# Optimization experiments

Hardware: AMD Instinct MI355X
Metric: run time of the kernel (lower is better)

The kernel has to match this reference:

```python
import jax, jax.numpy as jnp
import numpy as np
from jax import lax

B, CI, CO, H, W = 2, 256, 256, 128, 128
K = 3
K2 = K * K  # 9 kernel taps
BN_EPS = 1e-5


def setup_inputs() -> dict:
    key = jax.random.key(0)
    ks = jax.random.split(key, 9)
    x = jax.random.normal(ks[0], (B, CI, H, W), jnp.float32)
    # conv_offset_mask: Conv2d(chi, 3*K2, 3, stride=1, pad=1) -> [o_y/o_x interleaved (2*K2) | mask (K2)]
    w_off = jax.random.normal(ks[1], (3 * K2, CI, K, K), jnp.float32) * 0.01
    b_off = jax.random.normal(ks[2], (3 * K2,), jnp.float32) * 0.01
    # modulated deformable conv weight/bias
    w_dcn = jax.random.normal(ks[3], (CO, CI, K, K), jnp.float32) * (1.0 / np.float32(np.sqrt(CI * K2)))
    b_dcn = jax.random.normal(ks[4], (CO,), jnp.float32) * 0.01
    # BatchNorm2d (eval-mode affine + running stats)
    gamma = jax.random.uniform(ks[5], (CO,), jnp.float32, 0.5, 1.5)
    beta = jax.random.normal(ks[6], (CO,), jnp.float32) * 0.1
    run_mean = jax.random.normal(ks[7], (CO,), jnp.float32) * 0.1
    run_var = jax.random.uniform(ks[8], (CO,), jnp.float32, 0.5, 1.5)
    return {"x": x, "w_off": w_off, "b_off": b_off, "w_dcn": w_dcn,
            "b_dcn": b_dcn, "gamma": gamma, "beta": beta,
            "run_mean": run_mean, "run_var": run_var}


def _bilinear(x, py, px):
    """Sample x [B,C,H,W] at fractional coords (py,px) [B,H,W]; zero outside."""
    Bx, C, Hx, Wx = x.shape
    y0 = jnp.floor(py)
    x0 = jnp.floor(px)
    ly = py - y0
    lx = px - x0
    xf = x.reshape(Bx, C, Hx * Wx)

    def gather(yy, xx):
        valid = ((yy >= 0) & (yy <= Hx - 1) & (xx >= 0) & (xx <= Wx - 1)).astype(x.dtype)
        yi = jnp.clip(yy, 0, Hx - 1).astype(jnp.int32)
        xi = jnp.clip(xx, 0, Wx - 1).astype(jnp.int32)
        idx = (yi * Wx + xi).reshape(Bx, 1, Hx * Wx)
        v = jnp.take_along_axis(xf, idx, axis=2).reshape(Bx, C, Hx, Wx)
        return v * valid[:, None]

    w00 = ((1 - ly) * (1 - lx))[:, None]
    w01 = ((1 - ly) * lx)[:, None]
    w10 = (ly * (1 - lx))[:, None]
    w11 = (ly * lx)[:, None]
    return (w00 * gather(y0, x0) + w01 * gather(y0, x0 + 1)
            + w10 * gather(y0 + 1, x0) + w11 * gather(y0 + 1, x0 + 1))


def _deform_conv_bn_relu(x, w_off, b_off, w_dcn, b_dcn, gamma, beta, run_mean, run_var):
    # offset/mask predictor conv (stride 1, pad 1)
    om = lax.conv_general_dilated(x, w_off, (1, 1), ((1, 1), (1, 1))) + b_off[None, :, None, None]
    dy = om[:, 0:2 * K2:2]          # [B,K2,H,W]
    dx = om[:, 1:2 * K2:2]          # [B,K2,H,W]
    mask = jax.nn.sigmoid(om[:, 2 * K2:])  # [B,K2,H,W] modulation

    hh = jnp.arange(H, dtype=x.dtype)[:, None]  # [H,1]
    ww = jnp.arange(W, dtype=x.dtype)[None, :]  # [1,W]

    out = jnp.zeros((x.shape[0], w_dcn.shape[0], H, W), x.dtype)
    for k in range(K2):  # fixed small loop over the 9 kernel taps
        i, j = k // K, k % K
        py = hh - 1 + i + dy[:, k]  # pad=1, dilation=1
        px = ww - 1 + j + dx[:, k]
        val = _bilinear(x, py, px) * mask[:, k][:, None]  # [B,CI,H,W]
        out = out + jnp.einsum('oc,bchw->bohw', w_dcn[:, :, i, j], val)
    out = out + b_dcn[None, :, None, None]

    # BatchNorm2d (eval mode) + ReLU
    inv = gamma / jnp.sqrt(run_var + BN_EPS)
    out = out * inv[None, :, None, None] + (beta - run_mean * inv)[None, :, None, None]
    return jnp.maximum(out, 0.0)


def reference(x, w_off, b_off, w_dcn, b_dcn, gamma, beta, run_mean, run_var):
    return _deform_conv_bn_relu(x, w_off, b_off, w_dcn, b_dcn, gamma, beta, run_mean, run_var)
```

## Files before the change

### kernel.cpp

```cpp
#include <hip/hip_runtime.h>
#include <math.h>

#define Bn 2
#define CIc 256
#define COc 256
#define Hh 128
#define Ww 128
#define HW (Hh*Ww)

typedef unsigned short u16;
typedef unsigned int u32;
typedef __bf16 bf16x8 __attribute__((ext_vector_type(8)));
typedef float  f32x4  __attribute__((ext_vector_type(4)));
typedef float  f32x2  __attribute__((ext_vector_type(2)));
typedef u32    u32x4v __attribute__((ext_vector_type(4)));

#define WOFP_OFF  0
#define WPACK_OFF 36864
#define SCALE_OFF 331776
#define SHIFT_OFF 332032
#define XT_OFF    332288

__device__ __forceinline__ u16 f2bf(float f) {
    u32 u = __builtin_bit_cast(u32, f);
    return (u16)((u + 0x7FFFu + ((u >> 16) & 1u)) >> 16);
}
__device__ __forceinline__ u32 pkbf(float lo, float hi) {
    __bf16 a = (__bf16)lo, b = (__bf16)hi;
    return (u32)__builtin_bit_cast(u16, a) | ((u32)__builtin_bit_cast(u16, b) << 16);
}
__device__ __forceinline__ f32x2 unpk(u32 u) {
    f32x2 r;
    r.x = __builtin_bit_cast(float, u << 16);
    r.y = __builtin_bit_cast(float, u & 0xFFFF0000u);
    return r;
}

__global__ void prep_kernel(const float* __restrict__ w_off,
                            const float* __restrict__ w_dcn,
                            const float* __restrict__ b_dcn,
                            const float* __restrict__ gamma,
                            const float* __restrict__ beta,
                            const float* __restrict__ rmean,
                            const float* __restrict__ rvar,
                            float* __restrict__ ws) {
    int tid = blockIdx.x*blockDim.x + threadIdx.x;
    int nth = gridDim.x*blockDim.x;
    u16* wofp = (u16*)(ws + WOFP_OFF);
    u16* wpk  = (u16*)(ws + WPACK_OFF);
    for (int idx = tid; idx < 9*8*32*4*8; idx += nth) {
        int j = idx & 7, kb = (idx>>3)&3, co = (idx>>5)&31, s = (idx>>10)&7, k = idx>>13;
        int ci = kb*64 + s*8 + j;
        float v = (co < 27) ? w_off[(co*CIc + ci)*9 + k] : 0.f;
        wofp[idx] = f2bf(v);
    }
    for (int idx = tid; idx < 9*8*256*4*8; idx += nth) {
        int j = idx & 7, kb = (idx>>3)&3, co = (idx>>5)&255, s = (idx>>13)&7, k = idx>>16;
        int ci = kb*64 + s*8 + j;
        wpk[idx] = f2bf(w_dcn[(co*CIc + ci)*9 + k]);
    }
    if (tid < COc) {
        float inv = gamma[tid] * rsqrtf(rvar[tid] + 1e-5f);
        ws[SCALE_OFF+tid] = inv;
        ws[SHIFT_OFF+tid] = beta[tid] - rmean[tid]*inv + b_dcn[tid]*inv;
    }
}

__global__ __launch_bounds__(256) void transpose_kernel(const float* __restrict__ x,
                                                        float* __restrict__ ws) {
    __shared__ float tile[256][33];
    int bid = blockIdx.x;
    int b   = bid >> 9;
    int pxt = bid & 511;
    const float* xb = x + (size_t)b*CIc*HW + pxt*32;
    int px = threadIdx.x & 31, cg = threadIdx.x >> 5;
    #pragma unroll 8
    for (int it = 0; it < 32; it++) {
        int ci = it*8 + cg;
        tile[ci][px] = xb[(size_t)ci*HW + px];
    }
    __syncthreads();
    int px2 = threadIdx.x >> 3, oct = threadIdx.x & 7;
    u16* xto = (u16*)(ws + XT_OFF) + (((size_t)b*HW + pxt*32 + px2) << 8);
    #pragma unroll
    for (int uu = 0; uu < 4; uu++) {
        int u = uu*8 + oct;
        int cib = (u & 3)*64 + (u >> 2)*8;
        u32x4v v;
        #pragma unroll
        for (int t = 0; t < 4; t++)
            v[t] = pkbf(tile[cib + 2*t][px2], tile[cib + 2*t + 1][px2]);
        *(u32x4v*)(xto + u*8) = v;
    }
}

__device__ __forceinline__ void calc_corners(const float* spy, const float* spxs, const float* smk,
        int k, int p_s, int sub, const u16* xt,
        float& w00, float& w01, float& w10, float& w11,
        const u16*& x00, const u16*& x01, const u16*& x10, const u16*& x11) {
    float pyv = spy[k*64 + p_s], pxv = spxs[k*64 + p_s], mv = smk[k*64 + p_s];
    float y0f = floorf(pyv), x0f = floorf(pxv);
    float ly = pyv - y0f, lx = pxv - x0f;
    int y0 = (int)y0f, x0i = (int)x0f;
    int y1 = y0 + 1, x1i = x0i + 1;
    float wy0 = ((unsigned)y0  < Hh) ? (1.f-ly) : 0.f;
    float wy1 = ((unsigned)y1  < Hh) ? ly       : 0.f;
    float wx0 = ((unsigned)x0i < Ww) ? (1.f-lx) : 0.f;
    float wx1 = ((unsigned)x1i < Ww) ? lx       : 0.f;
    w00 = wy0*wx0*mv; w01 = wy0*wx1*mv; w10 = wy1*wx0*mv; w11 = wy1*wx1*mv;
    int cy0 = min(max(y0,0),Hh-1), cy1 = min(max(y1,0),Hh-1);
    int cx0 = min(max(x0i,0),Ww-1), cx1 = min(max(x1i,0),Ww-1);
    x00 = xt + ((((cy0<<7)+cx0)<<8) + sub*8);
    x01 = xt + ((((cy0<<7)+cx1)<<8) + sub*8);
    x10 = xt + ((((cy1<<7)+cx0)<<8) + sub*8);
    x11 = xt + ((((cy1<<7)+cx1)<<8) + sub*8);
}

#define LOADG(gg, ubase) \
    _Pragma("unroll") for (int t = 0; t < 2; t++) { \
        int o = ((ubase) + t) << 5; \
        gg[t][0] = *(const u32x4v*)(x00 + o); \
        gg[t][1] = *(const u32x4v*)(x01 + o); \
        gg[t][2] = *(const u32x4v*)(x10 + o); \
        gg[t][3] = *(const u32x4v*)(x11 + o); \
    }

#define CONSG(gg, ubase, dst) \
    _Pragma("unroll") for (int t = 0; t < 2; t++) { \
        u32x4v vv; \
        _Pragma("unroll") for (int w2 = 0; w2 < 4; w2++) { \
            f32x2 r = unpk(gg[t][0][w2])*w00 + unpk(gg[t][1][w2])*w01 \
                    + unpk(gg[t][2][w2])*w10 + unpk(gg[t][3][w2])*w11; \
            vv[w2] = pkbf(r.x, r.y); \
        } \
        u32 uoff = (((u32)((ubase) + t) << 6) | wsub) ^ wswz; \
        *(u32x4v*)((dst) + wrbase0 + uoff) = vv; \
    }

__global__ __launch_bounds__(256, 2) void fused_kernel(const float* __restrict__ b_off,
                                                       const float* __restrict__ ws,
                                                       float* __restrict__ out) {
    __shared__ __align__(16) char smem[65536 + 3*576*4];
    float* fin  = (float*)smem;
    float* spy  = (float*)(smem + 65536);
    float* spxs = spy + 576;
    float* smk  = spxs + 576;

    int tid = threadIdx.x;
    int bid = blockIdx.x;
    int tile = (bid & 7)*64 + (bid >> 3);
    int b = tile >> 8;
    int pixbase = (tile & 255) * 64;
    int h  = pixbase >> 7;
    int w0 = pixbase & 127;

    const u16* wofp = (const u16*)(ws + WOFP_OFF);
    const u16* wpk  = (const u16*)(ws + WPACK_OFF);
    const u16* xt   = (const u16*)(ws + XT_OFF) + (size_t)b*HW*256;

    int l  = tid & 63;
    int wv = tid >> 6;
    int kb = l >> 4;
    int pxl = l & 15;
    int aoff = pxl*32 + kb*8;

    {
        int pxa = wv*16 + pxl;
        f32x4 oa0 = {0.f,0.f,0.f,0.f}, oa1 = {0.f,0.f,0.f,0.f};
        #pragma unroll
        for (int k = 0; k < 9; k++) {
            int ky = k/3, kx = k - 3*ky;
            int y  = h + ky - 1;
            int xw = w0 + pxa + kx - 1;
            bool ok = ((unsigned)y < Hh) && ((unsigned)xw < Ww);
            const u16* brow = xt + (((y << 7) + xw) << 8);
            const u16* wk = wofp + k*8192;
            #pragma unroll
            for (int s = 0; s < 8; s++) {
                bf16x8 bf = {};
                if (ok) bf = *(const bf16x8*)(brow + s*32 + kb*8);
                bf16x8 a0 = *(const bf16x8*)(wk + s*1024 + aoff);
                bf16x8 a1 = *(const bf16x8*)(wk + s*1024 + 512 + aoff);
                oa0 = __builtin_amdgcn_mfma_f32_16x16x32_bf16(a0, bf, oa0, 0,0,0);
                oa1 = __builtin_amdgcn_mfma_f32_16x16x32_bf16(a1, bf, oa1, 0,0,0);
            }
        }
        #pragma unroll
        for (int r = 0; r < 4; r++) {
            fin[(kb*4 + r)*64 + pxa]      = oa0[r];
            fin[(16 + kb*4 + r)*64 + pxa] = oa1[r];
        }
    }
    __syncthreads();
    for (int idx = tid; idx < 576; idx += 256) {
        int k = idx >> 6, p = idx & 63;
        float dy = fin[(2*k)*64 + p]   + b_off[2*k];
        float dx = fin[(2*k+1)*64 + p] + b_off[2*k+1];
        float mv = fin[(18+k)*64 + p]  + b_off[18+k];
        spy[idx]  = (float)(h - 1 + k/3) + dy;
        spxs[idx] = (float)(w0 + p - 1 + k%3) + dx;
        smk[idx]  = 1.f/(1.f + __expf(-mv));
    }
    __syncthreads();

    int p_s = tid >> 2;
    int sub = tid & 3;
    u32 wrbase0 = (u32)p_s*512;
    u32 wsub = (u32)sub << 4;
    u32 wswz = (u32)(p_s & 7) << 4;
    u32 rswz = (u32)(pxl & 7) << 4;

    f32x4 acc[4][4];
    #pragma unroll
    for (int mi = 0; mi < 4; mi++)
        #pragma unroll
        for (int bq = 0; bq < 4; bq++)
            acc[mi][bq] = (f32x4){0.f,0.f,0.f,0.f};

    {
        float w00,w01,w10,w11; const u16 *x00,*x01,*x10,*x11;
        calc_corners(spy, spxs, smk, 0, p_s, sub, xt, w00,w01,w10,w11, x00,x01,x10,x11);
        u32x4v ga[2][4], gb[2][4];
        LOADG(ga, 0); LOADG(gb, 2);
        CONSG(ga, 0, smem); CONSG(gb, 2, smem);
        LOADG(ga, 4); LOADG(gb, 6);
        CONSG(ga, 4, smem); CONSG(gb, 6, smem);
    }

    bf16x8 apreA[4], apreB[4];
    #pragma unroll
    for (int mi = 0; mi < 4; mi++)
        apreA[mi] = *(const bf16x8*)(wpk + wv*2048 + aoff + mi*512);
    __syncthreads();

    for (int k = 0; k < 9; k++) {
        const char* base_r = smem + ((k & 1) << 15);
        char* base_w = smem + (((k + 1) & 1) << 15);
        const u16* wkbase   = wpk + k*65536 + wv*2048 + aoff;
        const u16* wkbase_n = wpk + (k == 8 ? 8 : k+1)*65536 + wv*2048 + aoff;

        bool stage = (k != 8);
        float w00,w01,w10,w11; const u16 *x00=xt,*x01=xt,*x10=xt,*x11=xt;
        if (stage)
            calc_corners(spy, spxs, smk, k+1, p_s, sub, xt, w00,w01,w10,w11, x00,x01,x10,x11);

        u32x4v g0[2][4], g1[2][4];
        #pragma unroll
        for (int s = 0; s < 8; s++) {
            const u16* ap = (s < 7) ? (wkbase + (s+1)*8192) : wkbase_n;
            #pragma unroll
            for (int mi = 0; mi < 4; mi++)
                apreB[mi] = *(const bf16x8*)(ap + mi*512);
            if (stage) {
                if (s == 0) { LOADG(g0, 0); }
                if (s == 1) { LOADG(g1, 2); }
                if (s == 4) { CONSG(g0, 0, base_w); LOADG(g0, 4); }
                if (s == 5) { CONSG(g1, 2, base_w); LOADG(g1, 6); }
            }
            __builtin_amdgcn_sched_barrier(0);
            __builtin_amdgcn_s_setprio(1);
            u32 inn = ((u32)(s*64 + kb*16)) ^ rswz;
            #pragma unroll
            for (int bq = 0; bq < 4; bq++) {
                bf16x8 bb = *(const bf16x8*)(base_r + (pxl + bq*16)*512 + inn);
                #pragma unroll
                for (int mi = 0; mi < 4; mi++)
                    acc[mi][bq] = __builtin_amdgcn_mfma_f32_16x16x32_bf16(apreA[mi], bb, acc[mi][bq], 0,0,0);
            }
            __builtin_amdgcn_s_setprio(0);
            #pragma unroll
            for (int mi = 0; mi < 4; mi++) apreA[mi] = apreB[mi];
        }
        if (stage) { CONSG(g0, 4, base_w); CONSG(g1, 6, base_w); }
        __syncthreads();
    }

    int rbase = kb*4;
    #pragma unroll
    for (int mi = 0; mi < 4; mi++) {
        #pragma unroll
        for (int r = 0; r < 4; r++) {
            int co = wv*64 + mi*16 + rbase + r;
            float sc = ws[SCALE_OFF+co], sh = ws[SHIFT_OFF+co];
            float* op = out + ((size_t)(b*COc + co))*HW + pixbase + pxl;
            #pragma unroll
            for (int bq = 0; bq < 4; bq++)
                op[bq*16] = fmaxf(acc[mi][bq][r]*sc + sh, 0.f);
        }
    }
}

extern "C" void kernel_launch(void* const* d_in, const int* in_sizes, int n_in,
                              void* d_out, int out_size, void* d_ws, size_t ws_size,
                              hipStream_t stream) {
    const float* x     = (const float*)d_in[0];
    const float* w_off = (const float*)d_in[1];
    const float* b_off = (const float*)d_in[2];
    const float* w_dcn = (const float*)d_in[3];
    const float* b_dcn = (const float*)d_in[4];
    const float* gamma = (const float*)d_in[5];
    const float* beta  = (const float*)d_in[6];
    const float* rmean = (const float*)d_in[7];
    const float* rvar  = (const float*)d_in[8];
    float* out = (float*)d_out;
    float* ws  = (float*)d_ws;

    prep_kernel<<<512, 256, 0, stream>>>(w_off, w_dcn, b_dcn, gamma, beta, rmean, rvar, ws);
    transpose_kernel<<<1024, 256, 0, stream>>>(x, ws);
    fused_kernel<<<512, 256, 0, stream>>>(b_off, ws, out);
}
```

Measured before the change: 113.2 us.

## Warp-specialize fused kernel into MFMA and bilinear-gather producer waves

Raises the block to 384 threads: four waves do only the MFMA GEMM while two extra producer waves compute bilinear corners, gather from the transposed input and write the next tap's bf16 tile into shared memory. The interleaved gather/convert work is removed from the compute waves. Weight prefetch becomes a two-deep double buffer. The cost is more threads per block and launch bounds of 3 blocks per CU, which tightens the register budget. Each producer thread now handles 16 channel groups per pixel and relies on the per-tap barrier for handoff.

```diff
diff --git a/kernel.cpp b/kernel.cpp
--- a/kernel.cpp
+++ b/kernel.cpp
@@ -94,11 +94,11 @@
     }
 }
 
-__device__ __forceinline__ void calc_corners(const float* spy, const float* spxs, const float* smk,
-        int k, int p_s, int sub, const u16* xt,
+__device__ __forceinline__ void corners(const float* spy, const float* spxs, const float* smk,
+        int k, int p,
         float& w00, float& w01, float& w10, float& w11,
-        const u16*& x00, const u16*& x01, const u16*& x10, const u16*& x11) {
-    float pyv = spy[k*64 + p_s], pxv = spxs[k*64 + p_s], mv = smk[k*64 + p_s];
+        u32& c00, u32& c01, u32& c10, u32& c11) {
+    float pyv = spy[k*64 + p], pxv = spxs[k*64 + p], mv = smk[k*64 + p];
     float y0f = floorf(pyv), x0f = floorf(pxv);
     float ly = pyv - y0f, lx = pxv - x0f;
     int y0 = (int)y0f, x0i = (int)x0f;
@@ -110,34 +110,33 @@
     w00 = wy0*wx0*mv; w01 = wy0*wx1*mv; w10 = wy1*wx0*mv; w11 = wy1*wx1*mv;
     int cy0 = min(max(y0,0),Hh-1), cy1 = min(max(y1,0),Hh-1);
     int cx0 = min(max(x0i,0),Ww-1), cx1 = min(max(x1i,0),Ww-1);
-    x00 = xt + ((((cy0<<7)+cx0)<<8) + sub*8);
-    x01 = xt + ((((cy0<<7)+cx1)<<8) + sub*8);
-    x10 = xt + ((((cy1<<7)+cx0)<<8) + sub*8);
-    x11 = xt + ((((cy1<<7)+cx1)<<8) + sub*8);
-}
-
-#define LOADG(gg, ubase) \
+    c00 = ((((u32)cy0<<7)+(u32)cx0)<<8);
+    c01 = ((((u32)cy0<<7)+(u32)cx1)<<8);
+    c10 = ((((u32)cy1<<7)+(u32)cx0)<<8);
+    c11 = ((((u32)cy1<<7)+(u32)cx1)<<8);
+}
+
+#define ISSUE2(g, rel) { \
     _Pragma("unroll") for (int t = 0; t < 2; t++) { \
-        int o = ((ubase) + t) << 5; \
-        gg[t][0] = *(const u32x4v*)(x00 + o); \
-        gg[t][1] = *(const u32x4v*)(x01 + o); \
-        gg[t][2] = *(const u32x4v*)(x10 + o); \
-        gg[t][3] = *(const u32x4v*)(x11 + o); \
-    }
-
-#define CONSG(gg, ubase, dst) \
+        u32 uo = (u32)(ubase + (rel) + t) * 8; \
+        g[t][0] = *(const u32x4v*)(xt + c00 + uo); \
+        g[t][1] = *(const u32x4v*)(xt + c01 + uo); \
+        g[t][2] = *(const u32x4v*)(xt + c10 + uo); \
+        g[t][3] = *(const u32x4v*)(xt + c11 + uo); \
+    } }
+
+#define CONS2(g, rel, dst) { \
     _Pragma("unroll") for (int t = 0; t < 2; t++) { \
         u32x4v vv; \
         _Pragma("unroll") for (int w2 = 0; w2 < 4; w2++) { \
-            f32x2 r = unpk(gg[t][0][w2])*w00 + unpk(gg[t][1][w2])*w01 \
-                    + unpk(gg[t][2][w2])*w10 + unpk(gg[t][3][w2])*w11; \
+            f32x2 r = unpk(g[t][0][w2])*w00 + unpk(g[t][1][w2])*w01 \
+                    + unpk(g[t][2][w2])*w10 + unpk(g[t][3][w2])*w11; \
             vv[w2] = pkbf(r.x, r.y); \
         } \
-        u32 uoff = (((u32)((ubase) + t) << 6) | wsub) ^ wswz; \
-        *(u32x4v*)((dst) + wrbase0 + uoff) = vv; \
-    }
-
-__global__ __launch_bounds__(256, 2) void fused_kernel(const float* __restrict__ b_off,
+        *(u32x4v*)((dst) + (u32)p_s*512 + (((u32)(ubase + (rel) + t) << 4) ^ wswz)) = vv; \
+    } }
+
+__global__ __launch_bounds__(384, 3) void fused_kernel(const float* __restrict__ b_off,
                                                        const float* __restrict__ ws,
                                                        float* __restrict__ out) {
     __shared__ __align__(16) char smem[65536 + 3*576*4];
@@ -164,7 +163,7 @@
     int pxl = l & 15;
     int aoff = pxl*32 + kb*8;
 
-    {
+    if (wv < 4) {
         int pxa = wv*16 + pxl;
         f32x4 oa0 = {0.f,0.f,0.f,0.f}, oa1 = {0.f,0.f,0.f,0.f};
         #pragma unroll
@@ -192,7 +191,7 @@
         }
     }
     __syncthreads();
-    for (int idx = tid; idx < 576; idx += 256) {
+    for (int idx = tid; idx < 576; idx += 384) {
         int k = idx >> 6, p = idx & 63;
         float dy = fin[(2*k)*64 + p]   + b_off[2*k];
         float dx = fin[(2*k+1)*64 + p] + b_off[2*k+1];
@@ -203,10 +202,9 @@
     }
     __syncthreads();
 
-    int p_s = tid >> 2;
-    int sub = tid & 3;
-    u32 wrbase0 = (u32)p_s*512;
-    u32 wsub = (u32)sub << 4;
+    int ptid = tid - 256;
+    int p_s = ptid >> 1;
+    int ubase = (ptid & 1) * 16;
     u32 wswz = (u32)(p_s & 7) << 4;
     u32 rswz = (u32)(pxl & 7) << 4;
 
@@ -217,75 +215,87 @@
         for (int bq = 0; bq < 4; bq++)
             acc[mi][bq] = (f32x4){0.f,0.f,0.f,0.f};
 
-    {
-        float w00,w01,w10,w11; const u16 *x00,*x01,*x10,*x11;
-        calc_corners(spy, spxs, smk, 0, p_s, sub, xt, w00,w01,w10,w11, x00,x01,x10,x11);
-        u32x4v ga[2][4], gb[2][4];
-        LOADG(ga, 0); LOADG(gb, 2);
-        CONSG(ga, 0, smem); CONSG(gb, 2, smem);
-        LOADG(ga, 4); LOADG(gb, 6);
-        CONSG(ga, 4, smem); CONSG(gb, 6, smem);
-    }
-
-    bf16x8 apreA[4], apreB[4];
-    #pragma unroll
-    for (int mi = 0; mi < 4; mi++)
-        apreA[mi] = *(const bf16x8*)(wpk + wv*2048 + aoff + mi*512);
+    bf16x8 apre[2][4];
+    u32x4v gA[2][4], gB[2][4];
+
+    if (wv >= 4) {
+        float w00,w01,w10,w11; u32 c00,c01,c10,c11;
+        corners(spy, spxs, smk, 0, p_s, w00,w01,w10,w11, c00,c01,c10,c11);
+        ISSUE2(gA, 0); ISSUE2(gB, 2);
+        CONS2(gA, 0, smem); ISSUE2(gA, 4);
+        CONS2(gB, 2, smem); ISSUE2(gB, 6);
+        CONS2(gA, 4, smem); ISSUE2(gA, 8);
+        CONS2(gB, 6, smem); ISSUE2(gB, 10);
+        CONS2(gA, 8, smem); ISSUE2(gA, 12);
+        CONS2(gB, 10, smem); ISSUE2(gB, 14);
+        CONS2(gA, 12, smem);
+        CONS2(gB, 14, smem);
+    } else {
+        const u16* ap0 = wpk + wv*2048 + aoff;
+        #pragma unroll
+        for (int mi = 0; mi < 4; mi++) {
+            apre[0][mi] = *(const bf16x8*)(ap0 + mi*512);
+            apre[1][mi] = *(const bf16x8*)(ap0 + 8192 + mi*512);
+        }
+    }
     __syncthreads();
 
     for (int k = 0; k < 9; k++) {
         const char* base_r = smem + ((k & 1) << 15);
         char* base_w = smem + (((k + 1) & 1) << 15);
-        const u16* wkbase   = wpk + k*65536 + wv*2048 + aoff;
-        const u16* wkbase_n = wpk + (k == 8 ? 8 : k+1)*65536 + wv*2048 + aoff;
-
-        bool stage = (k != 8);
-        float w00,w01,w10,w11; const u16 *x00=xt,*x01=xt,*x10=xt,*x11=xt;
-        if (stage)
-            calc_corners(spy, spxs, smk, k+1, p_s, sub, xt, w00,w01,w10,w11, x00,x01,x10,x11);
-
-        u32x4v g0[2][4], g1[2][4];
-        #pragma unroll
-        for (int s = 0; s < 8; s++) {
-            const u16* ap = (s < 7) ? (wkbase + (s+1)*8192) : wkbase_n;
+
+        if (wv < 4) {
+            const u16* wkb   = wpk + k*65536 + wv*2048 + aoff;
+            const u16* wkb_n = wpk + ((k < 8) ? (k+1) : 8)*65536 + wv*2048 + aoff;
             #pragma unroll
-            for (int mi = 0; mi < 4; mi++)
-                apreB[mi] = *(const bf16x8*)(ap + mi*512);
-            if (stage) {
-                if (s == 0) { LOADG(g0, 0); }
-                if (s == 1) { LOADG(g1, 2); }
-                if (s == 4) { CONSG(g0, 0, base_w); LOADG(g0, 4); }
-                if (s == 5) { CONSG(g1, 2, base_w); LOADG(g1, 6); }
+            for (int s = 0; s < 8; s++) {
+                __builtin_amdgcn_sched_barrier(0);
+                __builtin_amdgcn_s_setprio(1);
+                u32 inn = ((u32)(s*64 + kb*16)) ^ rswz;
+                #pragma unroll
+                for (int bq = 0; bq < 4; bq++) {
+                    bf16x8 bb = *(const bf16x8*)(base_r + (pxl + bq*16)*512 + inn);
+                    #pragma unroll
+                    for (int mi = 0; mi < 4; mi++)
+                        acc[mi][bq] = __builtin_amdgcn_mfma_f32_16x16x32_bf16(apre[s&1][mi], bb, acc[mi][bq], 0,0,0);
+                }
+                __builtin_amdgcn_s_setprio(0);
+                if (k < 8 || s < 6) {
+                    const u16* ap = (s < 6) ? (wkb + (s+2)*8192) : (wkb_n + (s-6)*8192);
+                    #pragma unroll
+                    for (int mi = 0; mi < 4; mi++)
+                        apre[s&1][mi] = *(const bf16x8*)(ap + mi*512);
+                }
             }
-            __builtin_amdgcn_sched_barrier(0);
-            __builtin_amdgcn_s_setprio(1);
-            u32 inn = ((u32)(s*64 + kb*16)) ^ rswz;
+        } else if (k < 8) {
+            float w00,w01,w10,w11; u32 c00,c01,c10,c11;
+            corners(spy, spxs, smk, k+1, p_s, w00,w01,w10,w11, c00,c01,c10,c11);
+            ISSUE2(gA, 0); ISSUE2(gB, 2);
+            CONS2(gA, 0, base_w); ISSUE2(gA, 4);
+            CONS2(gB, 2, base_w); ISSUE2(gB, 6);
+            CONS2(gA, 4, base_w); ISSUE2(gA, 8);
+            CONS2(gB, 6, base_w); ISSUE2(gB, 10);
+            CONS2(gA, 8, base_w); ISSUE2(gA, 12);
+            CONS2(gB, 10, base_w); ISSUE2(gB, 14);
+            CONS2(gA, 12, base_w);
+            CONS2(gB, 14, base_w);
+        }
+        __syncthreads();
+    }
+
+    if (wv < 4) {
+        int rbase = kb*4;
+        #pragma unroll
+        for (int mi = 0; mi < 4; mi++) {
             #pragma unroll
-            for (int bq = 0; bq < 4; bq++) {
-                bf16x8 bb = *(const bf16x8*)(base_r + (pxl + bq*16)*512 + inn);
+            for (int r = 0; r < 4; r++) {
+                int co = wv*64 + mi*16 + rbase + r;
+                float sc = ws[SCALE_OFF+co], sh = ws[SHIFT_OFF+co];
+                float* op = out + ((size_t)(b*COc + co))*HW + pixbase + pxl;
                 #pragma unroll
-                for (int mi = 0; mi < 4; mi++)
-                    acc[mi][bq] = __builtin_amdgcn_mfma_f32_16x16x32_bf16(apreA[mi], bb, acc[mi][bq], 0,0,0);
+                for (int bq = 0; bq < 4; bq++)
+                    op[bq*16] = fmaxf(acc[mi][bq][r]*sc + sh, 0.f);
             }
-            __builtin_amdgcn_s_setprio(0);
-            #pragma unroll
-            for (int mi = 0; mi < 4; mi++) apreA[mi] = apreB[mi];
-        }
-        if (stage) { CONSG(g0, 4, base_w); CONSG(g1, 6, base_w); }
-        __syncthreads();
-    }
-
-    int rbase = kb*4;
-    #pragma unroll
-    for (int mi = 0; mi < 4; mi++) {
-        #pragma unroll
-        for (int r = 0; r < 4; r++) {
-            int co = wv*64 + mi*16 + rbase + r;
-            float sc = ws[SCALE_OFF+co], sh = ws[SHIFT_OFF+co];
-            float* op = out + ((size_t)(b*COc + co))*HW + pixbase + pxl;
-            #pragma unroll
-            for (int bq = 0; bq < 4; bq++)
-                op[bq*16] = fmaxf(acc[mi][bq][r]*sc + sh, 0.f);
         }
     }
 }
@@ -307,5 +317,5 @@
 
     prep_kernel<<<512, 256, 0, stream>>>(w_off, w_dcn, b_dcn, gamma, beta, rmean, rvar, ws);
     transpose_kernel<<<1024, 256, 0, stream>>>(x, ws);
-    fused_kernel<<<512, 256, 0, stream>>>(b_off, ws, out);
-}
+    fused_kernel<<<512, 384, 0, stream>>>(b_off, ws, out);
+}
```

Result: slower. 217.4 us (+92.1%).
